# Performance work log

Hardware: AMD Instinct MI355X
Metric: run time of the kernel (lower is better)

Reference implementation:

```python
import jax, jax.numpy as jnp
import numpy as np

N = 50000          # nodes
E = 800000         # edges (avg degree 16)
IN = 256           # in_feats
H = 8              # num_heads
DH = 32            # out_feats // num_heads
NE = 8             # num_etypes
ALPHA = 0.2        # LeakyReLU slope


def setup_inputs() -> dict:
    key = jax.random.key(0)
    ks = jax.random.split(key, 10)
    feat = jax.random.normal(ks[0], (N, IN), dtype=jnp.float32)
    src = jax.random.randint(ks[1], (E,), 0, N, dtype=jnp.int32)
    dst = jax.random.randint(ks[2], (E,), 0, N, dtype=jnp.int32)
    etype_ids = jax.random.randint(ks[3], (E,), 0, NE, dtype=jnp.int32)
    # learned parameters (xavier-ish scale)
    W_fc = jax.random.normal(ks[4], (IN, H * DH), dtype=jnp.float32) * 0.05
    b_fc = jnp.zeros((H * DH,), dtype=jnp.float32)
    edge_emb = jax.random.normal(ks[5], (NE, H * DH), dtype=jnp.float32) * 0.05
    attn = jax.random.normal(ks[6], (1, H, 3 * DH), dtype=jnp.float32) * 0.05
    W_res = jax.random.normal(ks[7], (IN, H * DH), dtype=jnp.float32) * 0.05
    b_res = jnp.zeros((H * DH,), dtype=jnp.float32)
    return {"feat": feat, "src": src, "dst": dst, "etype_ids": etype_ids,
            "W_fc": W_fc, "b_fc": b_fc, "edge_emb": edge_emb, "attn": attn,
            "W_res": W_res, "b_res": b_res}


def reference(feat, src, dst, etype_ids, W_fc, b_fc, edge_emb, attn, W_res, b_res):
    n = feat.shape[0]
    h = (feat @ W_fc + b_fc).reshape(n, H, DH)            # [N,H,d]
    e = edge_emb[etype_ids].reshape(-1, H, DH)            # [E,H,d]
    # attn dot over concat([h_src, h_dst, e]) decomposes into 3 partial dots
    a_src = attn[0, :, :DH]
    a_dst = attn[0, :, DH:2 * DH]
    a_e = attn[0, :, 2 * DH:]
    s_src = jnp.einsum('nhd,hd->nh', h, a_src)            # [N,H]
    s_dst = jnp.einsum('nhd,hd->nh', h, a_dst)            # [N,H]
    s_e = jnp.einsum('ehd,hd->eh', e, a_e)                # [E,H]
    score = jax.nn.leaky_relu(s_src[src] + s_dst[dst] + s_e, ALPHA)  # [E,H]
    # edge softmax over incoming edges of each dst node
    mx = jax.ops.segment_max(score, dst, num_segments=n)  # [N,H]
    ex = jnp.exp(score - mx[dst])                         # [E,H]
    den = jax.ops.segment_sum(ex, dst, num_segments=n)    # [N,H]
    w = ex / den[dst]                                     # [E,H]
    # scatter-sum weighted source features to destinations
    msg = h[src] * w[:, :, None]                          # [E,H,d]
    out = jax.ops.segment_sum(msg, dst, num_segments=n).reshape(n, H * DH)
    out = out + feat @ W_res + b_res                      # residual
    return jax.nn.elu(out)
```

## Files before the change

kernel.cpp:

```cpp
#include <hip/hip_runtime.h>
#include <hip/hip_bf16.h>
#include <cstdint>

#define NN 50000
#define NEDGE 800000
#define IND 256
#define NH 8
#define DHH 32
#define NET 8
#define LALPHA 0.2f
#define OD 256
#define CD 512
#define SCAN_BLOCKS 196
#define NBG 782
#define NBH 782

typedef __attribute__((ext_vector_type(8))) short short8;
typedef __attribute__((ext_vector_type(4))) float f32x4;
typedef __attribute__((ext_vector_type(4))) float f4v;
typedef __attribute__((ext_vector_type(2))) unsigned u2v;
typedef __attribute__((ext_vector_type(2))) int i2v;
typedef __attribute__((ext_vector_type(4))) int i4v;

__device__ __forceinline__ unsigned short f2bf(float x) {
  union { float f; unsigned u; } v; v.f = x;
  unsigned r = v.u + 0x7FFFu + ((v.u >> 16) & 1u);
  return (unsigned short)(r >> 16);
}
__device__ __forceinline__ float bf2f(unsigned short u) {
  union { unsigned u; float f; } v; v.u = ((unsigned)u) << 16;
  return v.f;
}
__device__ __forceinline__ float u2f_lo(unsigned w) {
  union { unsigned u; float f; } v; v.u = w << 16; return v.f;
}
__device__ __forceinline__ float u2f_hi(unsigned w) {
  union { unsigned u; float f; } v; v.u = w & 0xffff0000u; return v.f;
}

__global__ __launch_bounds__(256) void k_prep(const float* __restrict__ Wfc,
                                              const float* __restrict__ Wres,
                                              unsigned short* __restrict__ Wtb) {
  int id = blockIdx.x * 256 + threadIdx.x;
  int k = id >> 9;
  int c = id & 511;
  float v = (c < OD) ? Wfc[k * OD + c] : Wres[k * OD + (c - OD)];
  Wtb[(size_t)c * IND + k] = f2bf(v);
}

__global__ __launch_bounds__(256, 4) void k_gemm(const float* __restrict__ Af,
                                                 const unsigned short* __restrict__ Bt,
                                                 const float* __restrict__ bfc,
                                                 const float* __restrict__ bres,
                                                 const float* __restrict__ attn,
                                                 const int* __restrict__ dst,
                                                 int* __restrict__ cnt,
                                                 int* __restrict__ rk,
                                                 unsigned short* __restrict__ Hb,
                                                 unsigned short* __restrict__ Rb,
                                                 float* __restrict__ ssrc,
                                                 float* __restrict__ sdst) {
  __shared__ unsigned short Bs[64][264];
  int tid = threadIdx.x;

  if (blockIdx.x >= NBG) {
    int e0 = ((blockIdx.x - NBG) * 256 + tid) << 2;
    if (e0 < NEDGE) {
      i4v d4 = __builtin_nontemporal_load(reinterpret_cast<const i4v*>(dst + e0));
      i4v rv;
      rv.x = atomicAdd(&cnt[d4.x], 1);
      rv.y = atomicAdd(&cnt[d4.y], 1);
      rv.z = atomicAdd(&cnt[d4.z], 1);
      rv.w = atomicAdd(&cnt[d4.w], 1);
      __builtin_nontemporal_store(rv, reinterpret_cast<i4v*>(rk + e0));
    }
    return;
  }

  int wave = tid >> 6, lane = tid & 63;
  int row0 = blockIdx.x * 64;

  int sr = tid >> 2;
  int sc = (tid & 3) * 8;

  int arow = row0 + wave * 16 + (lane & 15);
  int lrow = arow < NN ? arow : NN - 1;
  int akof = (lane >> 4) * 8;
  short8 areg[8];
#pragma unroll
  for (int ks = 0; ks < 8; ++ks) {
    const float* p = Af + (size_t)lrow * IND + ks * 32 + akof;
    float4 f0 = *reinterpret_cast<const float4*>(p);
    float4 f1 = *reinterpret_cast<const float4*>(p + 4);
    unsigned short t8[8] = {f2bf(f0.x), f2bf(f0.y), f2bf(f0.z), f2bf(f0.w),
                            f2bf(f1.x), f2bf(f1.y), f2bf(f1.z), f2bf(f1.w)};
    areg[ks] = *reinterpret_cast<short8*>(t8);
  }

  int rl = wave * 16 + ((lane >> 4) * 4);
  int cl = lane & 15;

  for (int bn = 0; bn < 8; ++bn) {
    if (bn) __syncthreads();
#pragma unroll
    for (int j = 0; j < 8; ++j) {
      int k = j * 32 + sc;
      short8 bv = *reinterpret_cast<const short8*>(Bt + (size_t)(bn * 64 + sr) * IND + k);
      *reinterpret_cast<short8*>(&Bs[sr][k]) = bv;
    }
    __syncthreads();

    f32x4 acc[4];
#pragma unroll
    for (int i = 0; i < 4; ++i) acc[i] = (f32x4){0.f, 0.f, 0.f, 0.f};
#pragma unroll
    for (int ks = 0; ks < 8; ++ks) {
#pragma unroll
      for (int nf = 0; nf < 4; ++nf) {
        short8 b = *reinterpret_cast<const short8*>(&Bs[nf * 16 + cl][ks * 32 + akof]);
        acc[nf] = __builtin_amdgcn_mfma_f32_16x16x32_bf16(areg[ks], b, acc[nf], 0, 0, 0);
      }
    }

    bool isH = (bn < 4);
    float s0[4] = {0.f, 0.f, 0.f, 0.f}, s1[4] = {0.f, 0.f, 0.f, 0.f};
    float d0[4] = {0.f, 0.f, 0.f, 0.f}, d1[4] = {0.f, 0.f, 0.f, 0.f};
#pragma unroll
    for (int nf = 0; nf < 4; ++nf) {
      int gcol = bn * 64 + nf * 16 + cl;
      float bias = isH ? bfc[gcol] : bres[gcol - OD];
      float as_ = 0.f, ad_ = 0.f;
      if (isH) {
        int hh = gcol >> 5, dd = gcol & 31;
        as_ = attn[hh * 96 + dd];
        ad_ = attn[hh * 96 + 32 + dd];
      }
#pragma unroll
      for (int r = 0; r < 4; ++r) {
        int grow = row0 + rl + r;
        float vv = acc[nf][r] + bias;
        if (grow < NN) {
          if (isH) Hb[(size_t)grow * OD + gcol] = f2bf(vv);
          else Rb[(size_t)grow * OD + (gcol - OD)] = f2bf(vv);
        }
        if (isH) {
          if (nf < 2) { s0[r] = fmaf(vv, as_, s0[r]); d0[r] = fmaf(vv, ad_, d0[r]); }
          else        { s1[r] = fmaf(vv, as_, s1[r]); d1[r] = fmaf(vv, ad_, d1[r]); }
        }
      }
    }
    if (isH) {
      int h0 = 2 * bn, h1 = 2 * bn + 1;
#pragma unroll
      for (int r = 0; r < 4; ++r) {
        float vs0 = s0[r], vd0 = d0[r], vs1 = s1[r], vd1 = d1[r];
#pragma unroll
        for (int m = 8; m; m >>= 1) {
          vs0 += __shfl_xor(vs0, m, 16);
          vd0 += __shfl_xor(vd0, m, 16);
          vs1 += __shfl_xor(vs1, m, 16);
          vd1 += __shfl_xor(vd1, m, 16);
        }
        int grow = row0 + rl + r;
        if (cl == 0 && grow < NN) {
          ssrc[grow * NH + h0] = vs0;
          ssrc[grow * NH + h1] = vs1;
          sdst[grow * NH + h0] = vd0;
          sdst[grow * NH + h1] = vd1;
        }
      }
    }
  }
}

__global__ __launch_bounds__(256) void k_scanA(const int* __restrict__ cnt,
                                               int* __restrict__ off,
                                               int* __restrict__ bsum) {
  __shared__ int sh[256];
  int tid = threadIdx.x;
  int gi = blockIdx.x * 256 + tid;
  int c = (gi < NN) ? cnt[gi] : 0;
  sh[tid] = c;
  __syncthreads();
#pragma unroll
  for (int d = 1; d < 256; d <<= 1) {
    int v = (tid >= d) ? sh[tid - d] : 0;
    __syncthreads();
    sh[tid] += v;
    __syncthreads();
  }
  off[gi] = sh[tid] - c;
  if (tid == 255) bsum[blockIdx.x] = sh[255];
}

__global__ __launch_bounds__(256) void k_scanB_se(const int* __restrict__ bsum,
                                                  int* __restrict__ boff,
                                                  const float* __restrict__ ee,
                                                  const float* __restrict__ attn,
                                                  float* __restrict__ se) {
  __shared__ int sh[256];
  int tid = threadIdx.x;
  int c = (tid < SCAN_BLOCKS) ? bsum[tid] : 0;
  sh[tid] = c;
  __syncthreads();
#pragma unroll
  for (int d = 1; d < 256; d <<= 1) {
    int v = (tid >= d) ? sh[tid - d] : 0;
    __syncthreads();
    sh[tid] += v;
    __syncthreads();
  }
  boff[tid] = sh[tid] - c;
  int h = tid >> 5, dd = tid & 31;
  float ae = attn[h * 96 + 64 + dd];
  for (int et = 0; et < NET; ++et) {
    float p = ee[et * OD + tid] * ae;
#pragma unroll
    for (int off2 = 16; off2; off2 >>= 1) p += __shfl_xor(p, off2, 32);
    if (dd == 0) se[et * NH + h] = p;
  }
}

__global__ __launch_bounds__(256) void k_edge(const int* __restrict__ src,
                                              const int* __restrict__ dst,
                                              const int* __restrict__ ety,
                                              const int* __restrict__ rk,
                                              const float* __restrict__ ssrc,
                                              const float* __restrict__ sdst,
                                              const float* __restrict__ se,
                                              const int* __restrict__ off,
                                              const int* __restrict__ boff,
                                              int* __restrict__ recs) {
  __shared__ float sse[64];
  int tid = threadIdx.x;
  if (tid < 64) sse[tid] = se[tid];
  __syncthreads();
  int t = blockIdx.x * 256 + tid;
  int e0 = t << 2;
  if (e0 >= NEDGE) return;
  i4v s4 = __builtin_nontemporal_load(reinterpret_cast<const i4v*>(src + e0));
  i4v d4 = __builtin_nontemporal_load(reinterpret_cast<const i4v*>(dst + e0));
  i4v t4 = __builtin_nontemporal_load(reinterpret_cast<const i4v*>(ety + e0));
  i4v r4 = __builtin_nontemporal_load(reinterpret_cast<const i4v*>(rk + e0));
#pragma unroll
  for (int j = 0; j < 4; ++j) {
    int u = (j == 0) ? s4.x : (j == 1) ? s4.y : (j == 2) ? s4.z : s4.w;
    int v = (j == 0) ? d4.x : (j == 1) ? d4.y : (j == 2) ? d4.z : d4.w;
    int et = (j == 0) ? t4.x : (j == 1) ? t4.y : (j == 2) ? t4.z : t4.w;
    int r = (j == 0) ? r4.x : (j == 1) ? r4.y : (j == 2) ? r4.z : r4.w;
    int pos = off[v] + boff[v >> 8] + r;
    float4 a0 = *reinterpret_cast<const float4*>(ssrc + (size_t)u * NH);
    float4 a1 = *reinterpret_cast<const float4*>(ssrc + (size_t)u * NH + 4);
    float4 b0 = *reinterpret_cast<const float4*>(sdst + (size_t)v * NH);
    float4 b1 = *reinterpret_cast<const float4*>(sdst + (size_t)v * NH + 4);
    float sa[8] = {a0.x + b0.x, a0.y + b0.y, a0.z + b0.z, a0.w + b0.w,
                   a1.x + b1.x, a1.y + b1.y, a1.z + b1.z, a1.w + b1.w};
    unsigned short w8[8];
#pragma unroll
    for (int h = 0; h < 8; ++h) {
      float s = sa[h] + sse[et * NH + h];
      s = s > 0.f ? s : LALPHA * s;
      w8[h] = f2bf(__expf(s));
    }
    int* rp = recs + (size_t)pos * 6;
    i2v hd; hd.x = u << 8; hd.y = 0;
    *reinterpret_cast<i2v*>(rp) = hd;
    ushort4 o0, o1;
    o0.x = w8[0]; o0.y = w8[1]; o0.z = w8[2]; o0.w = w8[3];
    o1.x = w8[4]; o1.y = w8[5]; o1.z = w8[6]; o1.w = w8[7];
    *reinterpret_cast<ushort4*>(rp + 2) = o0;
    *reinterpret_cast<ushort4*>(rp + 4) = o1;
  }
}

__global__ __launch_bounds__(256) void k_agg2(const unsigned short* __restrict__ Hb,
                                              const unsigned short* __restrict__ Rb,
                                              const int* __restrict__ off,
                                              const int* __restrict__ boff,
                                              const int* __restrict__ recs,
                                              float* __restrict__ out) {
  int v = blockIdx.x * 4 + (threadIdx.x >> 6);
  int lane = threadIdx.x & 63;
  if (v >= NN) return;
  int h = lane >> 3;
  int lo = off[v] + boff[v >> 8];
  int hi = off[v + 1] + boff[(v + 1) >> 8];
  unsigned lane4 = (unsigned)(lane << 2);
  float a0 = 0.f, a1 = 0.f, a2 = 0.f, a3 = 0.f, dsum = 0.f;
  const int* ri = recs + (size_t)lo * 6;
  const unsigned short* rs = reinterpret_cast<const unsigned short*>(ri);
  int n = hi - lo;
  int i = 0;
  for (; i + 4 <= n; i += 4) {
    unsigned o0 = (unsigned)ri[0] + lane4;
    unsigned o1 = (unsigned)ri[6] + lane4;
    unsigned o2 = (unsigned)ri[12] + lane4;
    unsigned o3 = (unsigned)ri[18] + lane4;
    float p0 = bf2f(rs[4 + h]);
    float p1 = bf2f(rs[16 + h]);
    float p2 = bf2f(rs[28 + h]);
    float p3 = bf2f(rs[40 + h]);
    u2v x0 = *reinterpret_cast<const u2v*>(Hb + o0);
    u2v x1 = *reinterpret_cast<const u2v*>(Hb + o1);
    u2v x2 = *reinterpret_cast<const u2v*>(Hb + o2);
    u2v x3 = *reinterpret_cast<const u2v*>(Hb + o3);
    a0 = fmaf(p0, u2f_lo(x0.x), a0); a1 = fmaf(p0, u2f_hi(x0.x), a1);
    a2 = fmaf(p0, u2f_lo(x0.y), a2); a3 = fmaf(p0, u2f_hi(x0.y), a3);
    a0 = fmaf(p1, u2f_lo(x1.x), a0); a1 = fmaf(p1, u2f_hi(x1.x), a1);
    a2 = fmaf(p1, u2f_lo(x1.y), a2); a3 = fmaf(p1, u2f_hi(x1.y), a3);
    a0 = fmaf(p2, u2f_lo(x2.x), a0); a1 = fmaf(p2, u2f_hi(x2.x), a1);
    a2 = fmaf(p2, u2f_lo(x2.y), a2); a3 = fmaf(p2, u2f_hi(x2.y), a3);
    a0 = fmaf(p3, u2f_lo(x3.x), a0); a1 = fmaf(p3, u2f_hi(x3.x), a1);
    a2 = fmaf(p3, u2f_lo(x3.y), a2); a3 = fmaf(p3, u2f_hi(x3.y), a3);
    dsum += (p0 + p1) + (p2 + p3);
    ri += 24; rs += 48;
  }
  for (; i < n; ++i) {
    unsigned o0 = (unsigned)ri[0] + lane4;
    float p0 = bf2f(rs[4 + h]);
    u2v x0 = *reinterpret_cast<const u2v*>(Hb + o0);
    a0 = fmaf(p0, u2f_lo(x0.x), a0); a1 = fmaf(p0, u2f_hi(x0.x), a1);
    a2 = fmaf(p0, u2f_lo(x0.y), a2); a3 = fmaf(p0, u2f_hi(x0.y), a3);
    dsum += p0;
    ri += 6; rs += 12;
  }
  unsigned oi32 = (unsigned)v * OD + lane4;
  u2v rv = __builtin_nontemporal_load(reinterpret_cast<const u2v*>(Rb + oi32));
  float inv = (dsum > 0.f) ? 1.f / dsum : 0.f;
  float o0 = fmaf(a0, inv, u2f_lo(rv.x));
  float o1 = fmaf(a1, inv, u2f_hi(rv.x));
  float o2 = fmaf(a2, inv, u2f_lo(rv.y));
  float o3 = fmaf(a3, inv, u2f_hi(rv.y));
  f4v wv;
  wv.x = o0 > 0.f ? o0 : expm1f(o0);
  wv.y = o1 > 0.f ? o1 : expm1f(o1);
  wv.z = o2 > 0.f ? o2 : expm1f(o2);
  wv.w = o3 > 0.f ? o3 : expm1f(o3);
  __builtin_nontemporal_store(wv, reinterpret_cast<f4v*>(out + (size_t)v * OD + lane4));
}

extern "C" void kernel_launch(void* const* d_in, const int* in_sizes, int n_in,
                              void* d_out, int out_size, void* d_ws, size_t ws_size,
                              hipStream_t stream) {
  const float* feat = (const float*)d_in[0];
  const int* src = (const int*)d_in[1];
  const int* dst = (const int*)d_in[2];
  const int* ety = (const int*)d_in[3];
  const float* Wfc = (const float*)d_in[4];
  const float* bfc = (const float*)d_in[5];
  const float* ee = (const float*)d_in[6];
  const float* attn = (const float*)d_in[7];
  const float* Wres = (const float*)d_in[8];
  const float* bres = (const float*)d_in[9];
  float* out = (float*)d_out;

  char* w = (char*)d_ws;
  unsigned short* Wtb   = (unsigned short*)w; w += (size_t)CD * IND * 2;
  unsigned short* Hb    = (unsigned short*)w; w += (size_t)NN * OD * 2;
  unsigned short* Rb    = (unsigned short*)w; w += (size_t)NN * OD * 2;
  float* ssrc = (float*)w; w += (size_t)NN * NH * 4;
  float* sdst = (float*)w; w += (size_t)NN * NH * 4;
  float* se   = (float*)w; w += 64 * 4;
  int* cnt    = (int*)w; w += (size_t)NN * 4;
  int* rk     = (int*)w; w += (size_t)NEDGE * 4;
  int* off    = (int*)w; w += (size_t)(SCAN_BLOCKS * 256) * 4;
  int* bsum   = (int*)w; w += 256 * 4;
  int* boff   = (int*)w; w += 256 * 4;
  int* recs   = (int*)w; w += (size_t)NEDGE * 24;

  hipMemsetAsync(cnt, 0, (size_t)NN * 4, stream);

  k_prep<<<(CD * IND) / 256, 256, 0, stream>>>(Wfc, Wres, Wtb);
  k_gemm<<<NBG + NBH, 256, 0, stream>>>(feat, Wtb, bfc, bres, attn,
                                        dst, cnt, rk, Hb, Rb, ssrc, sdst);
  k_scanA<<<SCAN_BLOCKS, 256, 0, stream>>>(cnt, off, bsum);
  k_scanB_se<<<1, 256, 0, stream>>>(bsum, boff, ee, attn, se);
  k_edge<<<(NEDGE / 4 + 255) / 256, 256, 0, stream>>>(src, dst, ety, rk, ssrc, sdst, se,
                                                      off, boff, recs);
  k_agg2<<<NN / 4, 256, 0, stream>>>(Hb, Rb, off, boff, recs, out);
}
```

Before: 197.5 us.

## Split edge pass into CSR scatter plus per-destination score kernel

The single edge-parallel kernel, which gathered source/destination scores and scattered 24-byte records to random CSR positions, is split in two. A scatter kernel now writes only a packed 4-byte (src<<8|etype) word to each CSR slot. A second kernel walks destinations in CSR order, computing the per-head exp scores with coalesced record writes and a single sdst load per node. This reduces random write traffic but adds a kernel launch, an extra 3.2 MB buffer round-trip, and narrow 2-byte stores.

```diff
diff --git a/kernel.cpp b/kernel.cpp
--- a/kernel.cpp
+++ b/kernel.cpp
@@ -19,7 +19,6 @@
 typedef __attribute__((ext_vector_type(4))) float f32x4;
 typedef __attribute__((ext_vector_type(4))) float f4v;
 typedef __attribute__((ext_vector_type(2))) unsigned u2v;
-typedef __attribute__((ext_vector_type(2))) int i2v;
 typedef __attribute__((ext_vector_type(4))) int i4v;
 
 __device__ __forceinline__ unsigned short f2bf(float x) {
@@ -221,10 +220,31 @@
   }
 }
 
-__global__ __launch_bounds__(256) void k_edge(const int* __restrict__ src,
-                                              const int* __restrict__ dst,
-                                              const int* __restrict__ ety,
-                                              const int* __restrict__ rk,
+__global__ __launch_bounds__(256) void k_scatter(const int* __restrict__ src,
+                                                 const int* __restrict__ dst,
+                                                 const int* __restrict__ ety,
+                                                 const int* __restrict__ rk,
+                                                 const int* __restrict__ off,
+                                                 const int* __restrict__ boff,
+                                                 int* __restrict__ csrp) {
+  int t = blockIdx.x * 256 + threadIdx.x;
+  int e0 = t << 2;
+  if (e0 >= NEDGE) return;
+  i4v s4 = __builtin_nontemporal_load(reinterpret_cast<const i4v*>(src + e0));
+  i4v d4 = __builtin_nontemporal_load(reinterpret_cast<const i4v*>(dst + e0));
+  i4v t4 = __builtin_nontemporal_load(reinterpret_cast<const i4v*>(ety + e0));
+  i4v r4 = __builtin_nontemporal_load(reinterpret_cast<const i4v*>(rk + e0));
+#pragma unroll
+  for (int j = 0; j < 4; ++j) {
+    int s = (j == 0) ? s4.x : (j == 1) ? s4.y : (j == 2) ? s4.z : s4.w;
+    int d = (j == 0) ? d4.x : (j == 1) ? d4.y : (j == 2) ? d4.z : d4.w;
+    int et = (j == 0) ? t4.x : (j == 1) ? t4.y : (j == 2) ? t4.z : t4.w;
+    int r = (j == 0) ? r4.x : (j == 1) ? r4.y : (j == 2) ? r4.z : r4.w;
+    csrp[off[d] + boff[d >> 8] + r] = (s << 8) | et;
+  }
+}
+
+__global__ __launch_bounds__(256) void k_edge(const int* __restrict__ csrp,
                                               const float* __restrict__ ssrc,
                                               const float* __restrict__ sdst,
                                               const float* __restrict__ se,
@@ -235,41 +255,27 @@
   int tid = threadIdx.x;
   if (tid < 64) sse[tid] = se[tid];
   __syncthreads();
-  int t = blockIdx.x * 256 + tid;
-  int e0 = t << 2;
-  if (e0 >= NEDGE) return;
-  i4v s4 = __builtin_nontemporal_load(reinterpret_cast<const i4v*>(src + e0));
-  i4v d4 = __builtin_nontemporal_load(reinterpret_cast<const i4v*>(dst + e0));
-  i4v t4 = __builtin_nontemporal_load(reinterpret_cast<const i4v*>(ety + e0));
-  i4v r4 = __builtin_nontemporal_load(reinterpret_cast<const i4v*>(rk + e0));
-#pragma unroll
-  for (int j = 0; j < 4; ++j) {
-    int u = (j == 0) ? s4.x : (j == 1) ? s4.y : (j == 2) ? s4.z : s4.w;
-    int v = (j == 0) ? d4.x : (j == 1) ? d4.y : (j == 2) ? d4.z : d4.w;
-    int et = (j == 0) ? t4.x : (j == 1) ? t4.y : (j == 2) ? t4.z : t4.w;
-    int r = (j == 0) ? r4.x : (j == 1) ? r4.y : (j == 2) ? r4.z : r4.w;
-    int pos = off[v] + boff[v >> 8] + r;
-    float4 a0 = *reinterpret_cast<const float4*>(ssrc + (size_t)u * NH);
-    float4 a1 = *reinterpret_cast<const float4*>(ssrc + (size_t)u * NH + 4);
-    float4 b0 = *reinterpret_cast<const float4*>(sdst + (size_t)v * NH);
-    float4 b1 = *reinterpret_cast<const float4*>(sdst + (size_t)v * NH + 4);
-    float sa[8] = {a0.x + b0.x, a0.y + b0.y, a0.z + b0.z, a0.w + b0.w,
-                   a1.x + b1.x, a1.y + b1.y, a1.z + b1.z, a1.w + b1.w};
-    unsigned short w8[8];
-#pragma unroll
-    for (int h = 0; h < 8; ++h) {
-      float s = sa[h] + sse[et * NH + h];
-      s = s > 0.f ? s : LALPHA * s;
-      w8[h] = f2bf(__expf(s));
-    }
-    int* rp = recs + (size_t)pos * 6;
-    i2v hd; hd.x = u << 8; hd.y = 0;
-    *reinterpret_cast<i2v*>(rp) = hd;
-    ushort4 o0, o1;
-    o0.x = w8[0]; o0.y = w8[1]; o0.z = w8[2]; o0.w = w8[3];
-    o1.x = w8[4]; o1.y = w8[5]; o1.z = w8[6]; o1.w = w8[7];
-    *reinterpret_cast<ushort4*>(rp + 2) = o0;
-    *reinterpret_cast<ushort4*>(rp + 4) = o1;
+  int v = blockIdx.x * 4 + (tid >> 6);
+  int lane = tid & 63;
+  int g = lane >> 3, h = lane & 7;
+  int lo = off[v] + boff[v >> 8];
+  int hi = off[v + 1] + boff[(v + 1) >> 8];
+  int n = hi - lo;
+  float sd = sdst[v * NH + h];
+  for (int i = 0; i < n; i += 8) {
+    int idx = i + g;
+    bool ok = idx < n;
+    int pk = csrp[lo + (ok ? idx : 0)];
+    int u = pk >> 8;
+    int et = pk & 255;
+    float s = ssrc[u * NH + h] + sd + sse[et * NH + h];
+    s = s > 0.f ? s : LALPHA * s;
+    float p = __expf(s);
+    if (ok) {
+      int* rp = recs + (size_t)(lo + idx) * 6;
+      if (h == 0) rp[0] = u << 8;
+      reinterpret_cast<unsigned short*>(rp)[4 + h] = f2bf(p);
+    }
   }
 }
 
@@ -366,6 +372,7 @@
   int* off    = (int*)w; w += (size_t)(SCAN_BLOCKS * 256) * 4;
   int* bsum   = (int*)w; w += 256 * 4;
   int* boff   = (int*)w; w += 256 * 4;
+  int* csrp   = (int*)w; w += (size_t)NEDGE * 4;
   int* recs   = (int*)w; w += (size_t)NEDGE * 24;
 
   hipMemsetAsync(cnt, 0, (size_t)NN * 4, stream);
@@ -375,7 +382,8 @@
                                         dst, cnt, rk, Hb, Rb, ssrc, sdst);
   k_scanA<<<SCAN_BLOCKS, 256, 0, stream>>>(cnt, off, bsum);
   k_scanB_se<<<1, 256, 0, stream>>>(bsum, boff, ee, attn, se);
-  k_edge<<<(NEDGE / 4 + 255) / 256, 256, 0, stream>>>(src, dst, ety, rk, ssrc, sdst, se,
-                                                      off, boff, recs);
+  k_scatter<<<(NEDGE / 4 + 255) / 256, 256, 0, stream>>>(src, dst, ety, rk,
+                                                         off, boff, csrp);
+  k_edge<<<NN / 4, 256, 0, stream>>>(csrp, ssrc, sdst, se, off, boff, recs);
   k_agg2<<<NN / 4, 256, 0, stream>>>(Hb, Rb, off, boff, recs, out);
 }
```

Result: no change. 195.3 us (-1.1%).
